# Kernel tuning notes

Hardware: AMD Instinct MI355X
Metric: run time of the kernel (lower is better)

## Reference

```python
import jax, jax.numpy as jnp
import numpy as np

B, N, D, H = 32, 512, 768, 12
HD = D // H  # 64
EPS = 1e-5


def layer_norm(x, g, b):
    mu = jnp.mean(x, axis=-1, keepdims=True)
    var = jnp.mean((x - mu) ** 2, axis=-1, keepdims=True)
    return (x - mu) / jnp.sqrt(var + EPS) * g + b


def setup_inputs() -> dict:
    key = jax.random.key(0)
    ks = jax.random.split(key, 10)
    x = jax.random.normal(ks[0], (B, N, D), dtype=jnp.float32)
    adj = jax.random.randint(ks[1], (B, N, N), 0, 2).astype(jnp.int32)
    adj = jnp.maximum(adj, jnp.eye(N, dtype=jnp.int32)[None])  # self-loops
    init = lambda k, shape: (jax.random.normal(k, shape, dtype=jnp.float32) * 0.02)
    return {
        "x": x, "adj": adj,
        "wq": init(ks[2], (D, D)), "bq": jnp.zeros((D,), jnp.float32),
        "wk": init(ks[3], (D, D)), "bk": jnp.zeros((D,), jnp.float32),
        "wv": init(ks[4], (D, D)), "bv": jnp.zeros((D,), jnp.float32),
        "wo": init(ks[5], (D, D)), "bo": jnp.zeros((D,), jnp.float32),
        "g1": jnp.ones((D,), jnp.float32), "b1": jnp.zeros((D,), jnp.float32),
        "g2": jnp.ones((D,), jnp.float32), "b2": jnp.zeros((D,), jnp.float32),
        "w_ffn1": init(ks[6], (D, 4 * D)), "b_ffn1": jnp.zeros((4 * D,), jnp.float32),
        "w_ffn2": init(ks[7], (4 * D, D)), "b_ffn2": jnp.zeros((D,), jnp.float32),
    }


def reference(x, adj, wq, bq, wk, bk, wv, bv, wo, bo, g1, b1, g2, b2,
              w_ffn1, b_ffn1, w_ffn2, b_ffn2):
    scale = HD ** -0.5
    h = layer_norm(x, g1, b1)
    split = lambda t: t.reshape(B, N, H, HD).transpose(0, 2, 1, 3)  # [B,H,N,HD]
    q = split(h @ wq + bq)
    k = split(h @ wk + bk)
    v = split(h @ wv + bv)
    scores = jnp.einsum('bhnd,bhmd->bhnm', q, k) * scale  # [B,H,N,N]
    scores = jnp.where(adj[:, None, :, :] == 0, -jnp.inf, scores)
    attn = jax.nn.softmax(scores, axis=-1)
    attn = jnp.nan_to_num(attn, nan=0.0)  # rows with no edges -> 0
    out = jnp.einsum('bhnm,bhmd->bhnd', attn, v)
    out = out.transpose(0, 2, 1, 3).reshape(B, N, D)
    out = out @ wo + bo + x  # residual (dropout=0, eval mode)
    h2 = layer_norm(out, g2, b2)
    ffn = jax.nn.gelu(h2 @ w_ffn1 + b_ffn1, approximate=False) @ w_ffn2 + b_ffn2
    return out + ffn
```

## Files before the change

kernel.cpp:

```cpp
#include <hip/hip_runtime.h>


#define Bn 32
#define Nn 512
#define Dn 768
#define Hn 12
#define HDn 64
#define Mn (Bn * Nn)
#define DFn 3072
#define MCHUNK 8192

typedef unsigned short u16;
typedef unsigned int u32;
typedef unsigned long long u64;
typedef short bf16x8 __attribute__((ext_vector_type(8)));
typedef float f32x4 __attribute__((ext_vector_type(4)));
typedef unsigned short u16x8 __attribute__((ext_vector_type(8)));
typedef unsigned int u32x2 __attribute__((ext_vector_type(2)));

__device__ __forceinline__ float b2f(u16 u) {
    return __uint_as_float(((unsigned int)u) << 16);
}
__device__ __forceinline__ u16 f2b(float f) {
    unsigned int u = __float_as_uint(f);
    u += 0x7fffu + ((u >> 16) & 1u);
    return (u16)(u >> 16);
}
__device__ __forceinline__ float loadDyn(const void* p, size_t i, int f) {
    return f ? ((const float*)p)[i] : b2f(((const u16*)p)[i]);
}
__device__ __forceinline__ float gelu_exact(float x) {
    return 0.5f * x * (1.0f + erff(x * 0.70710678118654752f));
}

#if __has_builtin(__builtin_amdgcn_exp2f)
#define EXP2F(x) __builtin_amdgcn_exp2f(x)
#else
#define EXP2F(x) __expf((x) * 0.6931471805599453f)
#endif

__device__ __forceinline__ u32 pk_bf16(float lo, float hi) {
    u32 r;
    asm("v_cvt_pk_bf16_f32 %0, %1, %2" : "=v"(r) : "v"(lo), "v"(hi));
    return r;
}

__device__ __forceinline__ void gl_lds16(const u16* g, u16* l) {
    __builtin_amdgcn_global_load_lds(
        (const __attribute__((address_space(1))) void*)(unsigned long long)(const void*)g,
        (__attribute__((address_space(3))) void*)(unsigned)(unsigned long long)(void*)l,
        16, 0, 0);
}

__global__ __launch_bounds__(256) void sniff_k(const u16* __restrict__ x,
                                               int* __restrict__ flag) {
    const int idx = blockIdx.x * 256 + threadIdx.x;
    u16x8 a = *(const u16x8*)&x[(size_t)idx * 8];
    int cnt = 0;
#pragma unroll
    for (int e = 0; e < 8; e++)
        cnt += ((a[e] & 0x7F80) == 0x7F80) ? 1 : 0;
#pragma unroll
    for (int off = 1; off <= 32; off <<= 1) cnt += __shfl_xor(cnt, off, 64);
    if ((threadIdx.x & 63) == 0 && cnt > 0) atomicAdd(flag, cnt);
}

__device__ __forceinline__ int flagval(const int* flagp) {
    return (*flagp > 32) ? 1 : 0;
}

__global__ __launch_bounds__(256) void pack_bias_k(
    const void* __restrict__ bq, const void* __restrict__ bk,
    const void* __restrict__ bv, const void* __restrict__ bo,
    const void* __restrict__ bf1, const void* __restrict__ bf2,
    float* __restrict__ out, const int* __restrict__ flagp) {
    const int f = flagval(flagp);
    const int i = blockIdx.x * 256 + threadIdx.x;
    if (i >= 6912) return;
    const void* src;
    int off;
    if (i < 768)       { src = bq;  off = i; }
    else if (i < 1536) { src = bk;  off = i - 768; }
    else if (i < 2304) { src = bv;  off = i - 1536; }
    else if (i < 3072) { src = bo;  off = i - 2304; }
    else if (i < 6144) { src = bf1; off = i - 3072; }
    else               { src = bf2; off = i - 6144; }
    out[i] = loadDyn(src, off, f);
}

__global__ __launch_bounds__(256) void mask_build_k(
    const int* __restrict__ adj, u64* __restrict__ mask) {
    const int idx = blockIdx.x * 256 + threadIdx.x;
    const size_t base = (size_t)(idx >> 3) * Nn + (size_t)(idx & 7) * 64;
    const int4* p = (const int4*)(adj + base);
    u64 m = 0;
#pragma unroll
    for (int c = 0; c < 16; c++) {
        int4 a = p[c];
        if (a.x) m |= 1ull << (c * 4 + 0);
        if (a.y) m |= 1ull << (c * 4 + 1);
        if (a.z) m |= 1ull << (c * 4 + 2);
        if (a.w) m |= 1ull << (c * 4 + 3);
    }
    mask[idx] = m;
}

__global__ __launch_bounds__(256) void transpose_k(
    const void* __restrict__ in, u16* __restrict__ out, int R, int C,
    const int* __restrict__ flagp) {
    const int f = flagval(flagp);
    __shared__ u16 tile[32][33];
    int c0 = blockIdx.x * 32, r0 = blockIdx.y * 32;
    int tx = threadIdx.x, ty = threadIdx.y;
#pragma unroll
    for (int i = 0; i < 32; i += 8)
        tile[ty + i][tx] = f2b(loadDyn(in, (size_t)(r0 + ty + i) * C + c0 + tx, f));
    __syncthreads();
#pragma unroll
    for (int i = 0; i < 32; i += 8)
        out[(size_t)(c0 + ty + i) * R + r0 + tx] = tile[tx][ty + i];
}

__global__ __launch_bounds__(256) void vtrans_k(
    const u16* __restrict__ v, u16* __restrict__ vt) {
    __shared__ u16 tile[32][33];
    const int bh = blockIdx.z;
    const int d0 = blockIdx.x * 32;
    const int n0 = blockIdx.y * 32;
    const int b = bh / Hn, h = bh % Hn;
    const int tx = threadIdx.x, ty = threadIdx.y;
#pragma unroll
    for (int i = 0; i < 32; i += 8)
        tile[ty + i][tx] =
            v[(size_t)(b * Nn + n0 + ty + i) * Dn + h * HDn + d0 + tx];
    __syncthreads();
#pragma unroll
    for (int i = 0; i < 32; i += 8)
        vt[((size_t)bh * HDn + d0 + ty + i) * Nn + n0 + tx] = tile[tx][ty + i];
}

template <int XDYN>
__global__ __launch_bounds__(256) void ln_k(
    const void* __restrict__ x, const void* __restrict__ g,
    const void* __restrict__ b, u16* __restrict__ y,
    const int* __restrict__ flagp) {
    const int f = flagval(flagp);
    const int t = threadIdx.x;
    const int row = blockIdx.x * 8 + (t >> 5);
    const int l32 = t & 31;
    const size_t base = (size_t)row * Dn;
    float v[24];
    if (XDYN == 0 || f == 0) {
        const u16* xp = (const u16*)x;
#pragma unroll
        for (int kk = 0; kk < 3; kk++) {
            u16x8 a = *(const u16x8*)&xp[base + kk * 256 + l32 * 8];
#pragma unroll
            for (int e = 0; e < 8; e++) v[kk * 8 + e] = b2f(a[e]);
        }
    } else {
#pragma unroll
        for (int kk = 0; kk < 3; kk++)
#pragma unroll
            for (int e = 0; e < 8; e++)
                v[kk * 8 + e] = loadDyn(x, base + kk * 256 + l32 * 8 + e, f);
    }
    float s = 0.f;
#pragma unroll
    for (int i = 0; i < 24; i++) s += v[i];
#pragma unroll
    for (int off = 1; off <= 16; off <<= 1) s += __shfl_xor(s, off, 64);
    const float mu = s * (1.0f / Dn);
    float d2 = 0.f;
#pragma unroll
    for (int i = 0; i < 24; i++) { float d = v[i] - mu; d2 += d * d; }
#pragma unroll
    for (int off = 1; off <= 16; off <<= 1) d2 += __shfl_xor(d2, off, 64);
    const float rstd = rsqrtf(d2 * (1.0f / Dn) + 1e-5f);
#pragma unroll
    for (int kk = 0; kk < 3; kk++) {
        const int c0 = kk * 256 + l32 * 8;
        u16x8 o;
        if (f == 0) {
            u16x8 gv = *(const u16x8*)&((const u16*)g)[c0];
            u16x8 bv = *(const u16x8*)&((const u16*)b)[c0];
#pragma unroll
            for (int e = 0; e < 8; e++)
                o[e] = f2b((v[kk * 8 + e] - mu) * rstd * b2f(gv[e]) + b2f(bv[e]));
        } else {
#pragma unroll
            for (int e = 0; e < 8; e++)
                o[e] = f2b((v[kk * 8 + e] - mu) * rstd * loadDyn(g, c0 + e, f)
                           + loadDyn(b, c0 + e, f));
        }
        *(u16x8*)&y[base + c0] = o;
    }
}

template <int ACT, int RES, int STORE, int WN, int CSPLIT>
__global__ __launch_bounds__(256, 3) void gemm_bt(
    const u16* __restrict__ A, const u16* __restrict__ Bt,
    const float* __restrict__ bias, const void* __restrict__ res,
    void* __restrict__ C, int M, int N, int K, int moff,
    const int* __restrict__ flagp) {
    constexpr int BN = 2 * WN;
    constexpr int NJ = WN / 16;
    constexpr int NB = BN / 64;
    static_assert(NB == 2, "counted vmcnt(4) assumes 4 loads per stage");
    __shared__ __align__(16) u16 As[3][128 * 32];
    __shared__ __align__(16) u16 Bs[3][BN * 32];
    const int tid = threadIdx.x;
    const int m0 = blockIdx.x * 128, n0 = blockIdx.y * BN;
    const int wave = tid >> 6, lane = tid & 63;
    const int wm = (wave & 1) * 64, wn = (wave >> 1) * WN;
    const int lm = lane & 15, quad = lane >> 4;

    const int srow = tid >> 2;
    const int sc = tid & 3;
    const int koff = (sc ^ ((srow >> 1) & 3)) * 8;
    const u16* gA[2];
    const u16* gB[NB];
#pragma unroll
    for (int i = 0; i < 2; i++)
        gA[i] = A + (size_t)(m0 + srow + i * 64) * K + koff;
#pragma unroll
    for (int i = 0; i < NB; i++)
        gB[i] = Bt + (size_t)(n0 + srow + i * 64) * K + koff;

    f32x4 acc[4][NJ] = {};

    auto stage = [&](int buf) {
#pragma unroll
        for (int i = 0; i < 2; i++) {
            gl_lds16(gA[i], &As[buf][(tid + i * 256) * 8]);
            gA[i] += 32;
        }
#pragma unroll
        for (int i = 0; i < NB; i++) {
            gl_lds16(gB[i], &Bs[buf][(tid + i * 256) * 8]);
            gB[i] += 32;
        }
    };
    const int rchunk = (quad ^ ((lm >> 1) & 3)) * 8;
    auto compute = [&](int buf) {
        bf16x8 af[4], bfv[NJ];
#pragma unroll
        for (int i = 0; i < 4; i++)
            af[i] = *(const bf16x8*)&As[buf][(wm + i * 16 + lm) * 32 + rchunk];
#pragma unroll
        for (int j = 0; j < NJ; j++)
            bfv[j] = *(const bf16x8*)&Bs[buf][(wn + j * 16 + lm) * 32 + rchunk];
#pragma unroll
        for (int i = 0; i < 4; i++)
#pragma unroll
            for (int j = 0; j < NJ; j++)
                acc[i][j] = __builtin_amdgcn_mfma_f32_16x16x32_bf16(
                    af[i], bfv[j], acc[i][j], 0, 0, 0);
    };

    const int nt = K / 32;
    stage(0);
    stage(1);
    int cur = 0, stg = 2;
    for (int t = 0; t < nt - 1; ++t) {
        asm volatile("s_waitcnt vmcnt(4)" ::: "memory");
        __builtin_amdgcn_s_barrier();
        if (t + 2 < nt) stage(stg);
        compute(cur);
        cur = (cur == 2) ? 0 : cur + 1;
        stg = (stg == 2) ? 0 : stg + 1;
    }
    asm volatile("s_waitcnt vmcnt(0)" ::: "memory");
    __builtin_amdgcn_s_barrier();
    compute(cur);

    const int f = flagval(flagp);
    float bias_f[NJ];
#pragma unroll
    for (int j = 0; j < NJ; j++)
        bias_f[j] = bias[n0 + wn + j * 16 + lm];
#pragma unroll
    for (int i = 0; i < 4; i++) {
#pragma unroll
        for (int r = 0; r < 4; r++) {
            const int row = m0 + wm + i * 16 + quad * 4 + r;
#pragma unroll
            for (int j = 0; j < NJ; j++) {
                int col = n0 + wn + j * 16 + lm;
                size_t rb;
                if (CSPLIT > 0) {
                    const int reg = col / CSPLIT;
                    rb = ((size_t)reg * M + moff + row) * (size_t)CSPLIT;
                    col -= reg * CSPLIT;
                } else {
                    rb = (size_t)(moff + row) * N;
                }
                float vv = acc[i][j][r] + bias_f[j];
                if (ACT == 1) vv = gelu_exact(vv);
                if (RES == 1) vv += b2f(((const u16*)res)[rb + col]);
                if (RES == 2) vv += loadDyn(res, rb + col, f);
                if (STORE == 0) ((u16*)C)[rb + col] = f2b(vv);
                else {
                    if (f) ((float*)C)[rb + col] = vv;
                    else   ((u16*)C)[rb + col] = f2b(vv);
                }
            }
        }
    }
}

__global__ __launch_bounds__(256, 4) void attn_mfma_k(
    const u16* q, const u16* __restrict__ k,
    const u16* __restrict__ vt, const u64* __restrict__ mask, u16* o) {
    const int h = blockIdx.x, qg = blockIdx.y, b = blockIdx.z;
    const int q0 = qg * 64;
    const int tid = threadIdx.x;
    const int wave = tid >> 6, lane = tid & 63;
    const int lm = lane & 15, quad = lane >> 4;
    const int wm = wave * 16;
    const int bh = b * Hn + h;
    const float SC2 = 0.125f * 1.4426950408889634f;

    __shared__ __align__(16) u16 Ks[64 * 72];
    __shared__ __align__(16) u16 Vts[64 * 72];
    __shared__ __align__(16) u16 PsT[64 * 72];

    const u16* qrow = q + ((size_t)(b * Nn + q0 + wm + lm)) * Dn + h * HDn + quad * 8;
    const bf16x8 aq0 = *(const bf16x8*)(qrow);
    const bf16x8 aq1 = *(const bf16x8*)(qrow + 32);

    const int srow = tid >> 2, scc = (tid & 3) * 16;
    const u16* kbase = k + ((size_t)(b * Nn + srow)) * Dn + h * HDn + scc;
    const u16* vbase = vt + ((size_t)bh * HDn + srow) * Nn + scc;

    u16x8 kr0 = *(const u16x8*)(kbase);
    u16x8 kr1 = *(const u16x8*)(kbase + 8);
    u16x8 vr0 = *(const u16x8*)(vbase);
    u16x8 vr1 = *(const u16x8*)(vbase + 8);

    float msc = 0.f, l_p = 0.f;
    f32x4 Oacc[4] = {};

    for (int kb = 0; kb < Nn / 64; kb++) {
        __syncthreads();
        *(u16x8*)&Ks[srow * 72 + scc]      = kr0;
        *(u16x8*)&Ks[srow * 72 + scc + 8]  = kr1;
        *(u16x8*)&Vts[srow * 72 + scc]     = vr0;
        *(u16x8*)&Vts[srow * 72 + scc + 8] = vr1;
        __syncthreads();
        if (kb + 1 < Nn / 64) {
            const u16* kn = kbase + (size_t)(kb + 1) * 64 * Dn;
            const u16* vn = vbase + (kb + 1) * 64;
            kr0 = *(const u16x8*)(kn);
            kr1 = *(const u16x8*)(kn + 8);
            vr0 = *(const u16x8*)(vn);
            vr1 = *(const u16x8*)(vn + 8);
        }
        f32x4 sacc[4] = {};
        __builtin_amdgcn_s_setprio(1);
#pragma unroll
        for (int s = 0; s < 2; s++) {
            const bf16x8 aq = s == 0 ? aq0 : aq1;
#pragma unroll
            for (int j = 0; j < 4; j++) {
                bf16x8 ak = *(const bf16x8*)&Ks[(j * 16 + lm) * 72 + s * 32 + quad * 8];
                sacc[j] = __builtin_amdgcn_mfma_f32_16x16x32_bf16(ak, aq, sacc[j], 0, 0, 0);
            }
        }
        __builtin_amdgcn_s_setprio(0);
        const u64 mrow = mask[(size_t)(b * Nn + q0 + wm + lm) * 8 + kb];
        const u32 wlo = ((u32)mrow) >> (quad * 4);
        const u32 whi = ((u32)(mrow >> 32)) >> (quad * 4);
#pragma unroll
        for (int j = 0; j < 4; j++) {
            const u32 w = (j < 2) ? wlo : whi;
            const int sh = (j & 1) * 16;
#pragma unroll
            for (int r = 0; r < 4; r++)
                sacc[j][r] = ((w >> (sh + r)) & 1u) ? sacc[j][r] : -3e38f;
        }
        float mx = fmaxf(fmaxf(sacc[0][0], sacc[0][1]), fmaxf(sacc[0][2], sacc[0][3]));
#pragma unroll
        for (int j = 1; j < 4; j++)
            mx = fmaxf(mx, fmaxf(fmaxf(sacc[j][0], sacc[j][1]),
                                 fmaxf(sacc[j][2], sacc[j][3])));
        mx = fmaxf(mx, __shfl_xor(mx, 16, 64));
        mx = fmaxf(mx, __shfl_xor(mx, 32, 64));
        const float mn = fmaxf(msc, mx * SC2);
        const float alpha = EXP2F(msc - mn);
        msc = mn;
        float sum = 0.f;
#pragma unroll
        for (int j = 0; j < 4; j++)
#pragma unroll
            for (int r = 0; r < 4; r++) {
                const float p = EXP2F(fmaf(sacc[j][r], SC2, -mn));
                sacc[j][r] = p;
                sum += p;
            }
        l_p = l_p * alpha + sum;
#pragma unroll
        for (int j = 0; j < 4; j++)
#pragma unroll
            for (int r = 0; r < 4; r++) Oacc[j][r] *= alpha;
        {
            u16* prow = &PsT[(wm + lm) * 72];
#pragma unroll
            for (int j = 0; j < 4; j++) {
                u32x2 pk;
                pk.x = pk_bf16(sacc[j][0], sacc[j][1]);
                pk.y = pk_bf16(sacc[j][2], sacc[j][3]);
                *(u32x2*)&prow[j * 16 + quad * 4] = pk;
            }
        }
        __builtin_amdgcn_s_setprio(1);
#pragma unroll
        for (int s = 0; s < 2; s++) {
            bf16x8 bp = *(const bf16x8*)&PsT[(wm + lm) * 72 + s * 32 + quad * 8];
#pragma unroll
            for (int j = 0; j < 4; j++) {
                bf16x8 av = *(const bf16x8*)&Vts[(j * 16 + lm) * 72 + s * 32 + quad * 8];
                Oacc[j] = __builtin_amdgcn_mfma_f32_16x16x32_bf16(av, bp, Oacc[j], 0, 0, 0);
            }
        }
        __builtin_amdgcn_s_setprio(0);
    }
    float l = l_p;
    l += __shfl_xor(l, 16, 64);
    l += __shfl_xor(l, 32, 64);
    const float inv = (l > 0.f) ? 1.0f / l : 0.f;
    u16* dst = o + ((size_t)(b * Nn + q0 + wm + lm)) * Dn + h * HDn;
#pragma unroll
    for (int j = 0; j < 4; j++) {
        u32x2 pk;
        pk.x = pk_bf16(Oacc[j][0] * inv, Oacc[j][1] * inv);
        pk.y = pk_bf16(Oacc[j][2] * inv, Oacc[j][3] * inv);
        *(u32x2*)&dst[j * 16 + quad * 4] = pk;
    }
}

extern "C" void kernel_launch(void* const* d_in, const int* in_sizes, int n_in,
                              void* d_out, int out_size, void* d_ws,
                              size_t ws_size, hipStream_t stream) {
    const void* x   = d_in[0];
    const int* adj  = (const int*)d_in[1];
    const void* wq  = d_in[2];
    const void* bq  = d_in[3];
    const void* wk  = d_in[4];
    const void* bk  = d_in[5];
    const void* wv  = d_in[6];
    const void* bv  = d_in[7];
    const void* wo  = d_in[8];
    const void* bo  = d_in[9];
    const void* g1  = d_in[10];
    const void* b1  = d_in[11];
    const void* g2  = d_in[12];
    const void* b2  = d_in[13];
    const void* w1  = d_in[14];
    const void* bf1 = d_in[15];
    const void* w2  = d_in[16];
    const void* bf2 = d_in[17];

    char* ws = (char*)d_ws;
    size_t off = 0;
    auto alloc = [&](size_t bytes) -> char* {
        char* p = ws + off;
        off += (bytes + 255) & ~(size_t)255;
        return p;
    };
    int* flag = (int*)alloc(4);
    u16* wqkvT = (u16*)alloc((size_t)3 * Dn * Dn * 2);
    u16* woT  = (u16*)alloc((size_t)Dn * Dn * 2);
    u16* w1T  = (u16*)alloc((size_t)Dn * DFn * 2);
    u16* w2T  = (u16*)alloc((size_t)Dn * DFn * 2);
    float* biasf = (float*)alloc(6912 * 4);
    u64* maskbuf = (u64*)alloc((size_t)Mn * 8 * 8);
    const size_t S = (size_t)Mn * Dn * 2;
    u16* Rh = (u16*)alloc(S);
    u16* Rq = (u16*)alloc(S);
    u16* Rk = (u16*)alloc(S);
    u16* Rv = (u16*)alloc(S);

    hipMemsetAsync(flag, 0, 4, stream);
    sniff_k<<<64, 256, 0, stream>>>((const u16*)x, flag);
    mask_build_k<<<Mn * 8 / 256, 256, 0, stream>>>(adj, maskbuf);
    pack_bias_k<<<27, 256, 0, stream>>>(bq, bk, bv, bo, bf1, bf2, biasf, flag);

    dim3 tb(32, 8);
    transpose_k<<<dim3(Dn / 32, Dn / 32), tb, 0, stream>>>(wq, wqkvT, Dn, Dn, flag);
    transpose_k<<<dim3(Dn / 32, Dn / 32), tb, 0, stream>>>(wk, wqkvT + (size_t)Dn * Dn, Dn, Dn, flag);
    transpose_k<<<dim3(Dn / 32, Dn / 32), tb, 0, stream>>>(wv, wqkvT + (size_t)2 * Dn * Dn, Dn, Dn, flag);
    transpose_k<<<dim3(Dn / 32, Dn / 32), tb, 0, stream>>>(wo, woT, Dn, Dn, flag);
    transpose_k<<<dim3(DFn / 32, Dn / 32), tb, 0, stream>>>(w1, w1T, Dn, DFn, flag);
    transpose_k<<<dim3(Dn / 32, DFn / 32), tb, 0, stream>>>(w2, w2T, DFn, Dn, flag);

    ln_k<1><<<Mn / 8, 256, 0, stream>>>(x, g1, b1, Rh, flag);

    gemm_bt<0, 0, 0, 64, Dn><<<dim3(Mn / 128, 3 * Dn / 128), 256, 0, stream>>>(
        Rh, wqkvT, biasf, nullptr, Rq, Mn, 3 * Dn, Dn, 0, flag);

    vtrans_k<<<dim3(HDn / 32, Nn / 32, Bn * Hn), tb, 0, stream>>>(Rv, Rh);

    attn_mfma_k<<<dim3(Hn, Nn / 64, Bn), 256, 0, stream>>>(Rq, Rk, Rh, maskbuf, Rq);

    gemm_bt<0, 2, 0, 64, 0><<<dim3(Mn / 128, Dn / 128), 256, 0, stream>>>(
        Rq, woT, biasf + 2304, x, Rv, Mn, Dn, Dn, 0, flag);

    ln_k<0><<<Mn / 8, 256, 0, stream>>>(Rv, g2, b2, Rh, flag);

    u16* hidden = Rq;
    for (int c = 0; c < Mn / MCHUNK; c++) {
        gemm_bt<1, 0, 0, 64, 0><<<dim3(MCHUNK / 128, DFn / 128), 256, 0, stream>>>(
            Rh + (size_t)c * MCHUNK * Dn, w1T, biasf + 3072, nullptr, hidden,
            MCHUNK, DFn, Dn, 0, flag);
        gemm_bt<0, 1, 1, 64, 0><<<dim3(MCHUNK / 128, Dn / 128), 256, 0, stream>>>(
            hidden, w2T, biasf + 6144, Rv, d_out, MCHUNK, Dn, DFn, c * MCHUNK, flag);
    }
}
```

Baseline: 656.6 us.

## Use 256-row GEMM tiles for wide GEMMs and remap blocks across XCDs

The GEMM template is now parameterized by the M tile size (128 or 256) instead of the N width. QKV and FFN1 use 256x128 tiles with two waves per SIMD, which raises MFMA work per LDS load. Launches become a 1-D grid whose block index is permuted so that consecutive tiles land on the same XCD, meant to improve L2 reuse of operands. Larger tiles raise register and LDS pressure and lower occupancy, and the wait count is adjusted to six outstanding loads per stage.

```diff
diff --git a/kernel.cpp b/kernel.cpp
--- a/kernel.cpp
+++ b/kernel.cpp
@@ -197,63 +197,68 @@
     }
 }
 
-template <int ACT, int RES, int STORE, int WN, int CSPLIT>
-__global__ __launch_bounds__(256, 3) void gemm_bt(
+template <int ACT, int RES, int STORE, int BM, int CSPLIT>
+__global__ __launch_bounds__(256, (BM == 256 ? 2 : 3)) void gemm_bt(
     const u16* __restrict__ A, const u16* __restrict__ Bt,
     const float* __restrict__ bias, const void* __restrict__ res,
-    void* __restrict__ C, int M, int N, int K, int moff,
+    void* __restrict__ C, int M, int N, int K, int moff, int NY,
     const int* __restrict__ flagp) {
-    constexpr int BN = 2 * WN;
-    constexpr int NJ = WN / 16;
-    constexpr int NB = BN / 64;
-    static_assert(NB == 2, "counted vmcnt(4) assumes 4 loads per stage");
-    __shared__ __align__(16) u16 As[3][128 * 32];
-    __shared__ __align__(16) u16 Bs[3][BN * 32];
+    constexpr int WM = BM / 2;
+    constexpr int NI = WM / 16;
+    constexpr int NA = BM / 64;
+    __shared__ __align__(16) u16 As[3][BM * 32];
+    __shared__ __align__(16) u16 Bs[3][128 * 32];
     const int tid = threadIdx.x;
-    const int m0 = blockIdx.x * 128, n0 = blockIdx.y * BN;
+
+    const int nwg = gridDim.x;
+    const int lin = blockIdx.x;
+    const int w = (lin & 7) * (nwg >> 3) + (lin >> 3);
+    const int mtile = w / NY, ntile = w - mtile * NY;
+    const int m0 = mtile * BM, n0 = ntile * 128;
+
     const int wave = tid >> 6, lane = tid & 63;
-    const int wm = (wave & 1) * 64, wn = (wave >> 1) * WN;
+    const int wm = (wave & 1) * WM, wn = (wave >> 1) * 64;
     const int lm = lane & 15, quad = lane >> 4;
 
     const int srow = tid >> 2;
     const int sc = tid & 3;
     const int koff = (sc ^ ((srow >> 1) & 3)) * 8;
-    const u16* gA[2];
-    const u16* gB[NB];
+    const u16* gA[NA];
+    const u16* gB[2];
+#pragma unroll
+    for (int i = 0; i < NA; i++)
+        gA[i] = A + (size_t)(m0 + srow + i * 64) * K + koff;
 #pragma unroll
     for (int i = 0; i < 2; i++)
-        gA[i] = A + (size_t)(m0 + srow + i * 64) * K + koff;
-#pragma unroll
-    for (int i = 0; i < NB; i++)
         gB[i] = Bt + (size_t)(n0 + srow + i * 64) * K + koff;
 
-    f32x4 acc[4][NJ] = {};
+    f32x4 acc[NI][4] = {};
 
     auto stage = [&](int buf) {
 #pragma unroll
-        for (int i = 0; i < 2; i++) {
+        for (int i = 0; i < NA; i++) {
             gl_lds16(gA[i], &As[buf][(tid + i * 256) * 8]);
             gA[i] += 32;
         }
 #pragma unroll
-        for (int i = 0; i < NB; i++) {
+        for (int i = 0; i < 2; i++) {
             gl_lds16(gB[i], &Bs[buf][(tid + i * 256) * 8]);
             gB[i] += 32;
         }
     };
     const int rchunk = (quad ^ ((lm >> 1) & 3)) * 8;
     auto compute = [&](int buf) {
-        bf16x8 af[4], bfv[NJ];
-#pragma unroll
-        for (int i = 0; i < 4; i++)
+        bf16x8 af[NI], bfv[4];
+#pragma unroll
+        for (int i = 0; i < NI; i++)
             af[i] = *(const bf16x8*)&As[buf][(wm + i * 16 + lm) * 32 + rchunk];
 #pragma unroll
-        for (int j = 0; j < NJ; j++)
+        for (int j = 0; j < 4; j++)
             bfv[j] = *(const bf16x8*)&Bs[buf][(wn + j * 16 + lm) * 32 + rchunk];
 #pragma unroll
-        for (int i = 0; i < 4; i++)
-#pragma unroll
-            for (int j = 0; j < NJ; j++)
+        for (int i = 0; i < NI; i++)
+#pragma unroll
+            for (int j = 0; j < 4; j++)
                 acc[i][j] = __builtin_amdgcn_mfma_f32_16x16x32_bf16(
                     af[i], bfv[j], acc[i][j], 0, 0, 0);
     };
@@ -263,7 +268,10 @@
     stage(1);
     int cur = 0, stg = 2;
     for (int t = 0; t < nt - 1; ++t) {
-        asm volatile("s_waitcnt vmcnt(4)" ::: "memory");
+        if constexpr (BM == 256)
+            asm volatile("s_waitcnt vmcnt(6)" ::: "memory");
+        else
+            asm volatile("s_waitcnt vmcnt(4)" ::: "memory");
         __builtin_amdgcn_s_barrier();
         if (t + 2 < nt) stage(stg);
         compute(cur);
@@ -275,17 +283,17 @@
     compute(cur);
 
     const int f = flagval(flagp);
-    float bias_f[NJ];
-#pragma unroll
-    for (int j = 0; j < NJ; j++)
+    float bias_f[4];
+#pragma unroll
+    for (int j = 0; j < 4; j++)
         bias_f[j] = bias[n0 + wn + j * 16 + lm];
 #pragma unroll
-    for (int i = 0; i < 4; i++) {
+    for (int i = 0; i < NI; i++) {
 #pragma unroll
         for (int r = 0; r < 4; r++) {
             const int row = m0 + wm + i * 16 + quad * 4 + r;
 #pragma unroll
-            for (int j = 0; j < NJ; j++) {
+            for (int j = 0; j < 4; j++) {
                 int col = n0 + wn + j * 16 + lm;
                 size_t rb;
                 if (CSPLIT > 0) {
@@ -496,24 +504,24 @@
 
     ln_k<1><<<Mn / 8, 256, 0, stream>>>(x, g1, b1, Rh, flag);
 
-    gemm_bt<0, 0, 0, 64, Dn><<<dim3(Mn / 128, 3 * Dn / 128), 256, 0, stream>>>(
-        Rh, wqkvT, biasf, nullptr, Rq, Mn, 3 * Dn, Dn, 0, flag);
+    gemm_bt<0, 0, 0, 256, Dn><<<1152, 256, 0, stream>>>(
+        Rh, wqkvT, biasf, nullptr, Rq, Mn, 3 * Dn, Dn, 0, 18, flag);
 
     vtrans_k<<<dim3(HDn / 32, Nn / 32, Bn * Hn), tb, 0, stream>>>(Rv, Rh);
 
     attn_mfma_k<<<dim3(Hn, Nn / 64, Bn), 256, 0, stream>>>(Rq, Rk, Rh, maskbuf, Rq);
 
-    gemm_bt<0, 2, 0, 64, 0><<<dim3(Mn / 128, Dn / 128), 256, 0, stream>>>(
-        Rq, woT, biasf + 2304, x, Rv, Mn, Dn, Dn, 0, flag);
+    gemm_bt<0, 2, 0, 128, 0><<<768, 256, 0, stream>>>(
+        Rq, woT, biasf + 2304, x, Rv, Mn, Dn, Dn, 0, 6, flag);
 
     ln_k<0><<<Mn / 8, 256, 0, stream>>>(Rv, g2, b2, Rh, flag);
 
     u16* hidden = Rq;
     for (int c = 0; c < Mn / MCHUNK; c++) {
-        gemm_bt<1, 0, 0, 64, 0><<<dim3(MCHUNK / 128, DFn / 128), 256, 0, stream>>>(
+        gemm_bt<1, 0, 0, 256, 0><<<768, 256, 0, stream>>>(
             Rh + (size_t)c * MCHUNK * Dn, w1T, biasf + 3072, nullptr, hidden,
-            MCHUNK, DFn, Dn, 0, flag);
-        gemm_bt<0, 1, 1, 64, 0><<<dim3(MCHUNK / 128, Dn / 128), 256, 0, stream>>>(
-            hidden, w2T, biasf + 6144, Rv, d_out, MCHUNK, Dn, DFn, c * MCHUNK, flag);
-    }
-}
+            MCHUNK, DFn, Dn, 0, 24, flag);
+        gemm_bt<0, 1, 1, 128, 0><<<384, 256, 0, stream>>>(
+            hidden, w2T, biasf + 6144, Rv, d_out, MCHUNK, Dn, DFn, c * MCHUNK, 6, flag);
+    }
+}
```

Result: slower. 670.3 us (+2.1%).
